# Kernel optimization log

Measured on AMD Instinct MI355X. Metric: run time of the kernel, lower is better.

Reference implementation:

```python
import jax, jax.numpy as jnp
import numpy as np

EMBED_DIM = 768
NUM_HEADS = 12
HEAD_DIM = EMBED_DIM // NUM_HEADS


def setup_inputs() -> dict:
    key = jax.random.key(0)
    k_x, k_wqkv, k_bqkv, k_wp, k_bp = jax.random.split(key, 5)
    B, S, D = 4, 2048, EMBED_DIM
    # nn.Linear default init scale ~ 1/sqrt(fan_in); exact distribution irrelevant for a reference
    lim = 1.0 / np.sqrt(D)
    x = jax.random.normal(k_x, (B, S, D), dtype=jnp.float32)
    w_qkv = jax.random.uniform(k_wqkv, (D, 3 * D), jnp.float32, -lim, lim)
    b_qkv = jax.random.uniform(k_bqkv, (3 * D,), jnp.float32, -lim, lim)
    w_proj = jax.random.uniform(k_wp, (D, D), jnp.float32, -lim, lim)
    b_proj = jax.random.uniform(k_bp, (D,), jnp.float32, -lim, lim)
    return {"x": x, "w_qkv": w_qkv, "b_qkv": b_qkv, "w_proj": w_proj, "b_proj": b_proj}


def reference(x, w_qkv, b_qkv, w_proj, b_proj):
    B, S, D = x.shape
    H, Hd = NUM_HEADS, HEAD_DIM
    qkv = x @ w_qkv + b_qkv                      # [B,S,3D]
    qkv = qkv.reshape(B, S, 3, H, Hd)
    qkv = jnp.transpose(qkv, (2, 0, 3, 1, 4))     # [3,B,H,S,Hd]
    q, k, v = qkv[0], qkv[1], qkv[2]
    scale = 1.0 / np.sqrt(Hd).astype(np.float32)
    scores = jnp.einsum("bhsd,bhtd->bhst", q, k) * scale  # [B,H,S,S]
    attn = jax.nn.softmax(scores, axis=-1)
    out = jnp.einsum("bhst,bhtd->bhsd", attn, v)  # [B,H,S,Hd]
    out = jnp.transpose(out, (0, 2, 1, 3)).reshape(B, S, D)
    return out @ w_proj + b_proj
```

## Files before the change

kernel.cpp:

```cpp
#include <hip/hip_runtime.h>


typedef _Float16 f16;
typedef _Float16 f16x8 __attribute__((ext_vector_type(8)));
typedef _Float16 f16x4 __attribute__((ext_vector_type(4)));
typedef float f32x4 __attribute__((ext_vector_type(4)));

#define BQ 4
#define SQ 2048
#define DQ 768
#define HQ 12
#define HD 64
#define M_TOK (BQ*SQ)
#define KVB 64
#define QSCALE 0.18033688f
#define THR_LOG2 11.5f

__device__ __forceinline__ void gld_lds16(const f16* g, f16* l) {
  __builtin_amdgcn_global_load_lds((const __attribute__((address_space(1))) void*)g,
                                   (__attribute__((address_space(3))) void*)l,
                                   16, 0, 0);
}

__global__ __launch_bounds__(256)
void prep(const float* __restrict__ x, f16* __restrict__ xh,
          const float* __restrict__ w_qkv, f16* __restrict__ wqkvT,
          const float* __restrict__ w_proj, f16* __restrict__ wprojT)
{
  __shared__ float tile[32][33];
  const int bid = blockIdx.x, tid = threadIdx.x;
  if (bid < 6144) {
    int i = (bid * 256 + tid) * 4;
    float4 v = *(const float4*)(x + i);
    f16x4 o = { (f16)v.x, (f16)v.y, (f16)v.z, (f16)v.w };
    *(f16x4*)(xh + i) = o;
    return;
  }
  const float* w; f16* wt; int K, N, nb, kb;
  if (bid < 7872) {
    int b2 = bid - 6144; w = w_qkv; wt = wqkvT; K = DQ; N = 3 * DQ;
    nb = (b2 % 72) * 32; kb = (b2 / 72) * 32;
  } else {
    int b3 = bid - 7872; w = w_proj; wt = wprojT; K = DQ; N = DQ;
    nb = (b3 % 24) * 32; kb = (b3 / 24) * 32;
  }
  int tx = tid & 31, ty = tid >> 5;
  for (int r = ty; r < 32; r += 8)
    tile[r][tx] = w[(size_t)(kb + r) * N + nb + tx];
  __syncthreads();
  for (int r = ty; r < 32; r += 8)
    wt[(size_t)(nb + r) * K + kb + tx] = (f16)tile[tx][r];
}

template<int MODE>
__global__ __launch_bounds__(256, 2)
void gemm128(const f16* __restrict__ A, const f16* __restrict__ Bt,
             const float* __restrict__ bias, float* __restrict__ Cf,
             f16* __restrict__ Qb, f16* __restrict__ Kb, f16* __restrict__ Vt,
             int M, int N, int K, int nbx)
{
  __shared__ f16 Ash[2][128 * 64];
  __shared__ f16 Bsh[2][128 * 64];
  const int tid = threadIdx.x;
  const int bid = blockIdx.x;
  const int nb = bid % nbx, mb = bid / nbx;
  const int m0 = mb * 128, n0 = nb * 128;
  const int lane = tid & 63, wid = tid >> 6;
  const int wr = wid >> 1, wc = wid & 1;
  const int l16 = lane & 15, l4 = lane >> 4;

  f32x4 acc[4][4] = {};

  const f16* aP[4]; const f16* bP[4]; int lOff[4];
  #pragma unroll
  for (int j = 0; j < 4; ++j) {
    int q = j * 256 + tid;
    int r = q >> 3;
    int sc = ((q & 7) ^ (r & 7)) * 8;
    aP[j] = A  + (size_t)(m0 + r) * K + sc;
    bP[j] = Bt + (size_t)(n0 + r) * K + sc;
    lOff[j] = q * 8;
  }

#define GSTAGE(buf, k0)                                   \
  do {                                                    \
    _Pragma("unroll")                                     \
    for (int j = 0; j < 4; ++j) {                         \
      gld_lds16(aP[j] + (k0), Ash[buf] + lOff[j]);        \
      gld_lds16(bP[j] + (k0), Bsh[buf] + lOff[j]);        \
    }                                                     \
  } while (0)

  GSTAGE(0, 0);
  __syncthreads();
  for (int k0 = 0; k0 < K; k0 += 64) {
    const int buf = (k0 >> 6) & 1;
    if (k0 + 64 < K) GSTAGE(buf ^ 1, k0 + 64);
    #pragma unroll
    for (int kk = 0; kk < 2; ++kk) {
      f16x8 af[4], bfr[4];
      #pragma unroll
      for (int m = 0; m < 4; ++m) {
        int R = wr * 64 + m * 16 + l16;
        af[m] = *(const f16x8*)(Ash[buf] + R * 64 + (((kk * 4 + l4) ^ (R & 7)) * 8));
      }
      #pragma unroll
      for (int n = 0; n < 4; ++n) {
        int R = wc * 64 + n * 16 + l16;
        bfr[n] = *(const f16x8*)(Bsh[buf] + R * 64 + (((kk * 4 + l4) ^ (R & 7)) * 8));
      }
      #pragma unroll
      for (int m = 0; m < 4; ++m)
        #pragma unroll
        for (int n = 0; n < 4; ++n)
          acc[m][n] = __builtin_amdgcn_mfma_f32_16x16x32_f16(af[m], bfr[n], acc[m][n], 0, 0, 0);
    }
    __syncthreads();
  }
#undef GSTAGE

  const int cbase = n0 + wc * 64;
  const int rbase = m0 + wr * 64;
  if (MODE == 1) {
    #pragma unroll
    for (int n = 0; n < 4; ++n) {
      int c = cbase + n * 16 + l16;
      float bv = bias[c];
      #pragma unroll
      for (int m = 0; m < 4; ++m)
        #pragma unroll
        for (int r = 0; r < 4; ++r) {
          int rr = rbase + m * 16 + l4 * 4 + r;
          Cf[(size_t)rr * N + c] = acc[m][n][r] + bv;
        }
    }
  } else {
    #pragma unroll
    for (int n = 0; n < 4; ++n) {
      int c = cbase + n * 16 + l16;
      float bv = bias[c];
      int which = c / DQ;
      int rem = c - which * DQ;
      int h = rem >> 6, hd = rem & 63;
      #pragma unroll
      for (int m = 0; m < 4; ++m) {
        int rr0 = rbase + m * 16 + l4 * 4;
        int b = rr0 >> 11, s = rr0 & 2047;
        size_t bh = (size_t)(b * HQ + h);
        if (which == 2) {
          f16x4 ov = { (f16)(acc[m][n][0] + bv), (f16)(acc[m][n][1] + bv),
                       (f16)(acc[m][n][2] + bv), (f16)(acc[m][n][3] + bv) };
          *(f16x4*)(Vt + (bh * HD + hd) * SQ + s) = ov;
        } else if (which == 0) {
          #pragma unroll
          for (int r = 0; r < 4; ++r)
            Qb[(bh * SQ + s + r) * HD + hd] = (f16)((acc[m][n][r] + bv) * QSCALE);
        } else {
          #pragma unroll
          for (int r = 0; r < 4; ++r)
            Kb[(bh * SQ + s + r) * HD + hd] = (f16)(acc[m][n][r] + bv);
        }
      }
    }
  }
}

__device__ __forceinline__ int permK(int p) {
  return ((p & 16) << 1) | (((p >> 2) & 3) << 3) | ((p & 32) >> 3) | (p & 3);
}

__global__ __launch_bounds__(256, 3)
void attn(const f16* __restrict__ Qb, const f16* __restrict__ Kb,
          const f16* __restrict__ Vt, f16* __restrict__ O)
{
  __shared__ f16 Ksh[2][KVB * HD];
  __shared__ f16 Vsh[2][HD * KVB];
  const int tid = threadIdx.x, lane = tid & 63, wid = tid >> 6;
  const int l16 = lane & 15, l4 = lane >> 4;

  const int nwg = gridDim.x;
  const int cpx = nwg >> 3;
  const int swz = (blockIdx.x & 7) * cpx + (blockIdx.x >> 3);
  const int qt = swz & 15, bh = swz >> 4;
  const int b = bh / HQ, h = bh - b * HQ;
  const f16* q  = Qb + (size_t)bh * SQ * HD;
  const f16* kp = Kb + (size_t)bh * SQ * HD;
  const f16* vp = Vt + (size_t)bh * HD * SQ;
  const int s0 = qt * 128 + wid * 32;

  f16x8 qf[2][2];
  #pragma unroll
  for (int g = 0; g < 2; ++g)
    #pragma unroll
    for (int kk = 0; kk < 2; ++kk)
      qf[g][kk] = *(const f16x8*)(q + (size_t)(s0 + g * 16 + l16) * HD + kk * 32 + l4 * 8);

  f32x4 oacc[2][4] = {};
  float mrun[2] = { -1e30f, -1e30f }, lrun[2] = { 0.f, 0.f };

  const int p0 = tid >> 3, p1 = (tid >> 3) + 32;
  const int scS = ((tid & 7) ^ (p0 & 7)) * 8;
  const int kr0 = permK(p0), kr1 = permK(p1);

#define STAGE(buf, t0)                                                        \
  do {                                                                        \
    gld_lds16(kp + (size_t)((t0) + kr0) * HD + scS, Ksh[buf] + tid * 8);      \
    gld_lds16(kp + (size_t)((t0) + kr1) * HD + scS, Ksh[buf] + (tid + 256) * 8);\
    gld_lds16(vp + (size_t)p0 * SQ + (t0) + scS,   Vsh[buf] + tid * 8);       \
    gld_lds16(vp + (size_t)p1 * SQ + (t0) + scS,   Vsh[buf] + (tid + 256) * 8);\
  } while (0)

#define COMPUTE(buf)                                                          \
  do {                                                                        \
    f32x4 sacc[2][4] = {};                                                    \
    __builtin_amdgcn_s_setprio(1);                                            \
    _Pragma("unroll")                                                         \
    for (int kk = 0; kk < 2; ++kk) {                                          \
      f16x8 kf[4];                                                            \
      _Pragma("unroll")                                                       \
      for (int n = 0; n < 4; ++n)                                             \
        kf[n] = *(const f16x8*)(Ksh[buf] + (n * 16 + l16) * HD +              \
                                ((kk * 32 + l4 * 8) ^ ((l16 & 7) * 8)));      \
      _Pragma("unroll")                                                       \
      for (int n = 0; n < 4; ++n) {                                           \
        sacc[0][n] = __builtin_amdgcn_mfma_f32_16x16x32_f16(kf[n], qf[0][kk], sacc[0][n], 0, 0, 0); \
        sacc[1][n] = __builtin_amdgcn_mfma_f32_16x16x32_f16(kf[n], qf[1][kk], sacc[1][n], 0, 0, 0); \
      }                                                                       \
    }                                                                         \
    __builtin_amdgcn_s_setprio(0);                                            \
    f16x8 bfr[2][2];                                                          \
    _Pragma("unroll")                                                         \
    for (int g = 0; g < 2; ++g) {                                             \
      float rm = -1e30f;                                                      \
      _Pragma("unroll")                                                       \
      for (int n = 0; n < 4; ++n)                                             \
        rm = fmaxf(rm, fmaxf(fmaxf(sacc[g][n][0], sacc[g][n][1]),             \
                             fmaxf(sacc[g][n][2], sacc[g][n][3])));           \
      rm = fmaxf(rm, __shfl_xor(rm, 16));                                     \
      rm = fmaxf(rm, __shfl_xor(rm, 32));                                     \
      if (!__all(rm - mrun[g] <= THR_LOG2)) {                                 \
        float mn = fmaxf(mrun[g], rm);                                        \
        float corr = __builtin_amdgcn_exp2f(mrun[g] - mn);                    \
        lrun[g] *= corr;                                                      \
        _Pragma("unroll")                                                     \
        for (int n = 0; n < 4; ++n)                                           \
          oacc[g][n] *= corr;                                                 \
        mrun[g] = mn;                                                         \
      }                                                                       \
      float mref = mrun[g];                                                   \
      float ps = 0.f;                                                         \
      _Pragma("unroll")                                                       \
      for (int n = 0; n < 4; ++n)                                             \
        _Pragma("unroll")                                                     \
        for (int r = 0; r < 4; ++r) {                                         \
          float pv = __builtin_amdgcn_exp2f(sacc[g][n][r] - mref);            \
          bfr[g][n & 1][(n >> 1) * 4 + r] = (f16)pv;                          \
          ps += pv;                                                           \
        }                                                                     \
      ps += __shfl_xor(ps, 16);                                               \
      ps += __shfl_xor(ps, 32);                                               \
      lrun[g] += ps;                                                          \
    }                                                                         \
    __builtin_amdgcn_s_setprio(1);                                            \
    _Pragma("unroll")                                                         \
    for (int kk = 0; kk < 2; ++kk) {                                          \
      f16x8 vf[4];                                                            \
      _Pragma("unroll")                                                       \
      for (int n = 0; n < 4; ++n)                                             \
        vf[n] = *(const f16x8*)(Vsh[buf] + (n * 16 + l16) * KVB +             \
                                ((kk * 32 + l4 * 8) ^ ((l16 & 7) * 8)));      \
      _Pragma("unroll")                                                       \
      for (int n = 0; n < 4; ++n) {                                           \
        oacc[0][n] = __builtin_amdgcn_mfma_f32_16x16x32_f16(vf[n], bfr[0][kk], oacc[0][n], 0, 0, 0); \
        oacc[1][n] = __builtin_amdgcn_mfma_f32_16x16x32_f16(vf[n], bfr[1][kk], oacc[1][n], 0, 0, 0); \
      }                                                                       \
    }                                                                         \
    __builtin_amdgcn_s_setprio(0);                                            \
  } while (0)

  STAGE(0, 0);
  __syncthreads();
  for (int t0 = 0; t0 < SQ; t0 += 2 * KVB) {
    STAGE(1, t0 + KVB);
    COMPUTE(0);
    __syncthreads();
    if (t0 + 2 * KVB < SQ) STAGE(0, t0 + 2 * KVB);
    COMPUTE(1);
    __syncthreads();
  }
#undef STAGE
#undef COMPUTE

  #pragma unroll
  for (int g = 0; g < 2; ++g) {
    float inv = 1.f / lrun[g];
    const int s = s0 + g * 16 + l16;
    f16* obase = O + ((size_t)b * SQ + s) * DQ + h * HD + l4 * 4;
    #pragma unroll
    for (int n = 0; n < 4; ++n) {
      f16x4 ov = { (f16)(oacc[g][n][0] * inv), (f16)(oacc[g][n][1] * inv),
                   (f16)(oacc[g][n][2] * inv), (f16)(oacc[g][n][3] * inv) };
      *(f16x4*)(obase + n * 16) = ov;
    }
  }
}

extern "C" void kernel_launch(void* const* d_in, const int* in_sizes, int n_in,
                              void* d_out, int out_size, void* d_ws, size_t ws_size,
                              hipStream_t stream) {
  const float* x      = (const float*)d_in[0];
  const float* w_qkv  = (const float*)d_in[1];
  const float* b_qkv  = (const float*)d_in[2];
  const float* w_proj = (const float*)d_in[3];
  const float* b_proj = (const float*)d_in[4];
  float* out = (float*)d_out;

  char* ws = (char*)d_ws;
  f16* xh     = (f16*)ws; ws += (size_t)M_TOK * DQ * 2;
  f16* wqkvT  = (f16*)ws; ws += (size_t)3 * DQ * DQ * 2;
  f16* wprojT = (f16*)ws; ws += (size_t)DQ * DQ * 2;
  f16* Qb     = (f16*)ws; ws += (size_t)M_TOK * DQ * 2;
  f16* Kb     = (f16*)ws; ws += (size_t)M_TOK * DQ * 2;
  f16* Vt     = (f16*)ws; ws += (size_t)M_TOK * DQ * 2;
  f16* AO     = xh;

  prep<<<8448, 256, 0, stream>>>(x, xh, w_qkv, wqkvT, w_proj, wprojT);

  gemm128<0><<<(M_TOK / 128) * (3 * DQ / 128), 256, 0, stream>>>(
      xh, wqkvT, b_qkv, nullptr, Qb, Kb, Vt, M_TOK, 3 * DQ, DQ, 3 * DQ / 128);

  attn<<<BQ * HQ * (SQ / 128), 256, 0, stream>>>(Qb, Kb, Vt, AO);

  gemm128<1><<<(M_TOK / 128) * (DQ / 128), 256, 0, stream>>>(
      AO, wprojT, b_proj, out, nullptr, nullptr, nullptr, M_TOK, DQ, DQ, DQ / 128);
}
```

Measured before the change: 160.0 us.

## Split attention KV range in two with a merge kernel; swizzle GEMM blocks

Attention now splits the key/value sequence into two halves, so the grid has twice as many workgroups. Each half writes partial fp32 outputs plus its running max and sum, and a new merge2 kernel combines them into the f16 output. The occupancy hint rises from 3 to 5 waves per SIMD, and the GEMM block index gets an XCD-style swizzle. This aims to fill the GPU better, but it adds a large fp32 partial write and read, an extra launch, and register pressure under the higher occupancy bound.

```diff
diff --git a/kernel.cpp b/kernel.cpp
--- a/kernel.cpp
+++ b/kernel.cpp
@@ -13,6 +13,7 @@
 #define HD 64
 #define M_TOK (BQ*SQ)
 #define KVB 64
+#define NROW (BQ*HQ*SQ)
 #define QSCALE 0.18033688f
 #define THR_LOG2 11.5f
 
@@ -62,7 +63,8 @@
   __shared__ f16 Ash[2][128 * 64];
   __shared__ f16 Bsh[2][128 * 64];
   const int tid = threadIdx.x;
-  const int bid = blockIdx.x;
+  const int cpx = gridDim.x >> 3;
+  const int bid = (blockIdx.x & 7) * cpx + (blockIdx.x >> 3);
   const int nb = bid % nbx, mb = bid / nbx;
   const int m0 = mb * 128, n0 = nb * 128;
   const int lane = tid & 63, wid = tid >> 6;
@@ -169,9 +171,11 @@
   return ((p & 16) << 1) | (((p >> 2) & 3) << 3) | ((p & 32) >> 3) | (p & 3);
 }
 
-__global__ __launch_bounds__(256, 3)
+template<int NSPLIT>
+__global__ __launch_bounds__(256, 5)
 void attn(const f16* __restrict__ Qb, const f16* __restrict__ Kb,
-          const f16* __restrict__ Vt, f16* __restrict__ O)
+          const f16* __restrict__ Vt, f16* __restrict__ O,
+          float* __restrict__ Po, float* __restrict__ Pm, float* __restrict__ Pl)
 {
   __shared__ f16 Ksh[2][KVB * HD];
   __shared__ f16 Vsh[2][HD * KVB];
@@ -181,7 +185,10 @@
   const int nwg = gridDim.x;
   const int cpx = nwg >> 3;
   const int swz = (blockIdx.x & 7) * cpx + (blockIdx.x >> 3);
-  const int qt = swz & 15, bh = swz >> 4;
+  int bh, qt, split;
+  if (NSPLIT == 2) { bh = swz >> 5; split = (swz >> 4) & 1; qt = swz & 15; }
+  else             { bh = swz >> 4; split = 0;              qt = swz & 15; }
+  const int tbase = split * (SQ / NSPLIT), tend = tbase + SQ / NSPLIT;
   const int b = bh / HQ, h = bh - b * HQ;
   const f16* q  = Qb + (size_t)bh * SQ * HD;
   const f16* kp = Kb + (size_t)bh * SQ * HD;
@@ -278,31 +285,69 @@
     __builtin_amdgcn_s_setprio(0);                                            \
   } while (0)
 
-  STAGE(0, 0);
+  STAGE(0, tbase);
   __syncthreads();
-  for (int t0 = 0; t0 < SQ; t0 += 2 * KVB) {
+  for (int t0 = tbase; t0 < tend; t0 += 2 * KVB) {
     STAGE(1, t0 + KVB);
     COMPUTE(0);
     __syncthreads();
-    if (t0 + 2 * KVB < SQ) STAGE(0, t0 + 2 * KVB);
+    if (t0 + 2 * KVB < tend) STAGE(0, t0 + 2 * KVB);
     COMPUTE(1);
     __syncthreads();
   }
 #undef STAGE
 #undef COMPUTE
 
-  #pragma unroll
-  for (int g = 0; g < 2; ++g) {
-    float inv = 1.f / lrun[g];
-    const int s = s0 + g * 16 + l16;
-    f16* obase = O + ((size_t)b * SQ + s) * DQ + h * HD + l4 * 4;
-    #pragma unroll
-    for (int n = 0; n < 4; ++n) {
-      f16x4 ov = { (f16)(oacc[g][n][0] * inv), (f16)(oacc[g][n][1] * inv),
-                   (f16)(oacc[g][n][2] * inv), (f16)(oacc[g][n][3] * inv) };
-      *(f16x4*)(obase + n * 16) = ov;
-    }
-  }
+  if (NSPLIT == 1) {
+    #pragma unroll
+    for (int g = 0; g < 2; ++g) {
+      float inv = 1.f / lrun[g];
+      const int s = s0 + g * 16 + l16;
+      f16* obase = O + ((size_t)b * SQ + s) * DQ + h * HD + l4 * 4;
+      #pragma unroll
+      for (int n = 0; n < 4; ++n) {
+        f16x4 ov = { (f16)(oacc[g][n][0] * inv), (f16)(oacc[g][n][1] * inv),
+                     (f16)(oacc[g][n][2] * inv), (f16)(oacc[g][n][3] * inv) };
+        *(f16x4*)(obase + n * 16) = ov;
+      }
+    }
+  } else {
+    #pragma unroll
+    for (int g = 0; g < 2; ++g) {
+      float inv = 1.f / lrun[g];
+      const int s = s0 + g * 16 + l16;
+      const size_t row = (size_t)split * NROW + (size_t)bh * SQ + s;
+      float* pb = Po + row * 64 + l4 * 4;
+      #pragma unroll
+      for (int n = 0; n < 4; ++n) {
+        float4 ov = { oacc[g][n][0] * inv, oacc[g][n][1] * inv,
+                      oacc[g][n][2] * inv, oacc[g][n][3] * inv };
+        *(float4*)(pb + n * 16) = ov;
+      }
+      if (l4 == 0) { Pm[row] = mrun[g]; Pl[row] = lrun[g]; }
+    }
+  }
+}
+
+__global__ __launch_bounds__(256)
+void merge2(const float* __restrict__ Po, const float* __restrict__ Pm,
+            const float* __restrict__ Pl, f16* __restrict__ AO)
+{
+  const int tid = threadIdx.x;
+  const int row = blockIdx.x * 4 + (tid >> 6);
+  const int e = tid & 63;
+  float m0 = Pm[row], m1 = Pm[row + NROW];
+  float l0 = Pl[row], l1 = Pl[row + NROW];
+  float m = fmaxf(m0, m1);
+  float w0 = l0 * __builtin_amdgcn_exp2f(m0 - m);
+  float w1 = l1 * __builtin_amdgcn_exp2f(m1 - m);
+  float inv = 1.f / (w0 + w1);
+  float o0 = Po[(size_t)row * 64 + e];
+  float o1 = Po[(size_t)(row + NROW) * 64 + e];
+  float o = (w0 * o0 + w1 * o1) * inv;
+  const int bh = row >> 11, s = row & 2047;
+  const int b = bh / HQ, h = bh - b * HQ;
+  AO[((size_t)(b * SQ + s)) * DQ + h * HD + e] = (f16)o;
 }
 
 extern "C" void kernel_launch(void* const* d_in, const int* in_sizes, int n_in,
@@ -322,14 +367,24 @@
   f16* Qb     = (f16*)ws; ws += (size_t)M_TOK * DQ * 2;
   f16* Kb     = (f16*)ws; ws += (size_t)M_TOK * DQ * 2;
   f16* Vt     = (f16*)ws; ws += (size_t)M_TOK * DQ * 2;
+  float* Po   = (float*)ws; ws += (size_t)2 * NROW * 64 * 4;
+  float* Pm   = (float*)ws; ws += (size_t)2 * NROW * 4;
+  float* Pl   = (float*)ws; ws += (size_t)2 * NROW * 4;
   f16* AO     = xh;
+
+  const bool use_split = ws_size >= (size_t)(ws - (char*)d_ws);
 
   prep<<<8448, 256, 0, stream>>>(x, xh, w_qkv, wqkvT, w_proj, wprojT);
 
   gemm128<0><<<(M_TOK / 128) * (3 * DQ / 128), 256, 0, stream>>>(
       xh, wqkvT, b_qkv, nullptr, Qb, Kb, Vt, M_TOK, 3 * DQ, DQ, 3 * DQ / 128);
 
-  attn<<<BQ * HQ * (SQ / 128), 256, 0, stream>>>(Qb, Kb, Vt, AO);
+  if (use_split) {
+    attn<2><<<BQ * HQ * (SQ / 128) * 2, 256, 0, stream>>>(Qb, Kb, Vt, AO, Po, Pm, Pl);
+    merge2<<<NROW / 4, 256, 0, stream>>>(Po, Pm, Pl, AO);
+  } else {
+    attn<1><<<BQ * HQ * (SQ / 128), 256, 0, stream>>>(Qb, Kb, Vt, AO, nullptr, nullptr, nullptr);
+  }
 
   gemm128<1><<<(M_TOK / 128) * (DQ / 128), 256, 0, stream>>>(
       AO, wprojT, b_proj, out, nullptr, nullptr, nullptr, M_TOK, DQ, DQ, DQ / 128);
```

After: 250.8 us. 56.8% more time.

## Interleave per-group softmax with PV MFMAs and swizzle GEMM block order

Applied to the files above, without the earlier changes.

The attention inner loop now loads all K and V fragments from LDS up front. It runs the softmax for group 0, issues that group's PV MFMAs, then runs group 1's softmax so it can overlap with the in-flight MFMAs instead of serializing both softmaxes before any PV work. The GEMM kernel also remaps block IDs in strides of eight, likely so neighbouring tiles land on the same XCD and share L2. The price is higher register pressure from holding kf/vf[2][4], which could hurt occupancy, and the remap assumes the grid size is a multiple of eight.

```diff
diff --git a/kernel.cpp b/kernel.cpp
--- a/kernel.cpp
+++ b/kernel.cpp
@@ -62,7 +62,8 @@
   __shared__ f16 Ash[2][128 * 64];
   __shared__ f16 Bsh[2][128 * 64];
   const int tid = threadIdx.x;
-  const int bid = blockIdx.x;
+  const int cpx = gridDim.x >> 3;
+  const int bid = (blockIdx.x & 7) * cpx + (blockIdx.x >> 3);
   const int nb = bid % nbx, mb = bid / nbx;
   const int m0 = mb * 128, n0 = nb * 128;
   const int lane = tid & 63, wid = tid >> 6;
@@ -210,71 +211,84 @@
     gld_lds16(vp + (size_t)p1 * SQ + (t0) + scS,   Vsh[buf] + (tid + 256) * 8);\
   } while (0)
 
+#define SOFTMAX(g)                                                            \
+  do {                                                                        \
+    float rm = -1e30f;                                                        \
+    _Pragma("unroll")                                                         \
+    for (int n = 0; n < 4; ++n)                                               \
+      rm = fmaxf(rm, fmaxf(fmaxf(sacc[g][n][0], sacc[g][n][1]),               \
+                           fmaxf(sacc[g][n][2], sacc[g][n][3])));             \
+    rm = fmaxf(rm, __shfl_xor(rm, 16));                                       \
+    rm = fmaxf(rm, __shfl_xor(rm, 32));                                       \
+    if (!__all(rm - mrun[g] <= THR_LOG2)) {                                   \
+      float mn = fmaxf(mrun[g], rm);                                          \
+      float corr = __builtin_amdgcn_exp2f(mrun[g] - mn);                      \
+      lrun[g] *= corr;                                                        \
+      _Pragma("unroll")                                                       \
+      for (int n = 0; n < 4; ++n)                                             \
+        oacc[g][n] *= corr;                                                   \
+      mrun[g] = mn;                                                           \
+    }                                                                         \
+    float mref = mrun[g];                                                     \
+    float ps = 0.f;                                                           \
+    _Pragma("unroll")                                                         \
+    for (int n = 0; n < 4; ++n)                                               \
+      _Pragma("unroll")                                                       \
+      for (int r = 0; r < 4; ++r) {                                           \
+        float pv = __builtin_amdgcn_exp2f(sacc[g][n][r] - mref);              \
+        bfr[g][n & 1][(n >> 1) * 4 + r] = (f16)pv;                            \
+        ps += pv;                                                             \
+      }                                                                       \
+    ps += __shfl_xor(ps, 16);                                                 \
+    ps += __shfl_xor(ps, 32);                                                 \
+    lrun[g] += ps;                                                            \
+  } while (0)
+
 #define COMPUTE(buf)                                                          \
   do {                                                                        \
     f32x4 sacc[2][4] = {};                                                    \
+    f16x8 kf[2][4];                                                           \
+    _Pragma("unroll")                                                         \
+    for (int kk = 0; kk < 2; ++kk)                                            \
+      _Pragma("unroll")                                                       \
+      for (int n = 0; n < 4; ++n)                                             \
+        kf[kk][n] = *(const f16x8*)(Ksh[buf] + (n * 16 + l16) * HD +          \
+                                    ((kk * 32 + l4 * 8) ^ ((l16 & 7) * 8)));  \
     __builtin_amdgcn_s_setprio(1);                                            \
     _Pragma("unroll")                                                         \
-    for (int kk = 0; kk < 2; ++kk) {                                          \
-      f16x8 kf[4];                                                            \
-      _Pragma("unroll")                                                       \
-      for (int n = 0; n < 4; ++n)                                             \
-        kf[n] = *(const f16x8*)(Ksh[buf] + (n * 16 + l16) * HD +              \
-                                ((kk * 32 + l4 * 8) ^ ((l16 & 7) * 8)));      \
-      _Pragma("unroll")                                                       \
-      for (int n = 0; n < 4; ++n) {                                           \
-        sacc[0][n] = __builtin_amdgcn_mfma_f32_16x16x32_f16(kf[n], qf[0][kk], sacc[0][n], 0, 0, 0); \
-        sacc[1][n] = __builtin_amdgcn_mfma_f32_16x16x32_f16(kf[n], qf[1][kk], sacc[1][n], 0, 0, 0); \
-      }                                                                       \
-    }                                                                         \
+    for (int kk = 0; kk < 2; ++kk)                                            \
+      _Pragma("unroll")                                                       \
+      for (int n = 0; n < 4; ++n)                                             \
+        sacc[0][n] = __builtin_amdgcn_mfma_f32_16x16x32_f16(kf[kk][n], qf[0][kk], sacc[0][n], 0, 0, 0); \
+    _Pragma("unroll")                                                         \
+    for (int kk = 0; kk < 2; ++kk)                                            \
+      _Pragma("unroll")                                                       \
+      for (int n = 0; n < 4; ++n)                                             \
+        sacc[1][n] = __builtin_amdgcn_mfma_f32_16x16x32_f16(kf[kk][n], qf[1][kk], sacc[1][n], 0, 0, 0); \
     __builtin_amdgcn_s_setprio(0);                                            \
+    f16x8 vf[2][4];                                                           \
+    _Pragma("unroll")                                                         \
+    for (int kk = 0; kk < 2; ++kk)                                            \
+      _Pragma("unroll")                                                       \
+      for (int n = 0; n < 4; ++n)                                             \
+        vf[kk][n] = *(const f16x8*)(Vsh[buf] + (n * 16 + l16) * KVB +         \
+                                    ((kk * 32 + l4 * 8) ^ ((l16 & 7) * 8)));  \
     f16x8 bfr[2][2];                                                          \
-    _Pragma("unroll")                                                         \
-    for (int g = 0; g < 2; ++g) {                                             \
-      float rm = -1e30f;                                                      \
-      _Pragma("unroll")                                                       \
-      for (int n = 0; n < 4; ++n)                                             \
-        rm = fmaxf(rm, fmaxf(fmaxf(sacc[g][n][0], sacc[g][n][1]),             \
-                             fmaxf(sacc[g][n][2], sacc[g][n][3])));           \
-      rm = fmaxf(rm, __shfl_xor(rm, 16));                                     \
-      rm = fmaxf(rm, __shfl_xor(rm, 32));                                     \
-      if (!__all(rm - mrun[g] <= THR_LOG2)) {                                 \
-        float mn = fmaxf(mrun[g], rm);                                        \
-        float corr = __builtin_amdgcn_exp2f(mrun[g] - mn);                    \
-        lrun[g] *= corr;                                                      \
-        _Pragma("unroll")                                                     \
-        for (int n = 0; n < 4; ++n)                                           \
-          oacc[g][n] *= corr;                                                 \
-        mrun[g] = mn;                                                         \
-      }                                                                       \
-      float mref = mrun[g];                                                   \
-      float ps = 0.f;                                                         \
-      _Pragma("unroll")                                                       \
-      for (int n = 0; n < 4; ++n)                                             \
-        _Pragma("unroll")                                                     \
-        for (int r = 0; r < 4; ++r) {                                         \
-          float pv = __builtin_amdgcn_exp2f(sacc[g][n][r] - mref);            \
-          bfr[g][n & 1][(n >> 1) * 4 + r] = (f16)pv;                          \
-          ps += pv;                                                           \
-        }                                                                     \
-      ps += __shfl_xor(ps, 16);                                               \
-      ps += __shfl_xor(ps, 32);                                               \
-      lrun[g] += ps;                                                          \
-    }                                                                         \
+    SOFTMAX(0);                    \
     __builtin_amdgcn_s_setprio(1);                                            \
     _Pragma("unroll")                                                         \
-    for (int kk = 0; kk < 2; ++kk) {                                          \
-      f16x8 vf[4];                                                            \
-      _Pragma("unroll")                                                       \
-      for (int n = 0; n < 4; ++n)                                             \
-        vf[n] = *(const f16x8*)(Vsh[buf] + (n * 16 + l16) * KVB +             \
-                                ((kk * 32 + l4 * 8) ^ ((l16 & 7) * 8)));      \
-      _Pragma("unroll")                                                       \
-      for (int n = 0; n < 4; ++n) {                                           \
-        oacc[0][n] = __builtin_amdgcn_mfma_f32_16x16x32_f16(vf[n], bfr[0][kk], oacc[0][n], 0, 0, 0); \
-        oacc[1][n] = __builtin_amdgcn_mfma_f32_16x16x32_f16(vf[n], bfr[1][kk], oacc[1][n], 0, 0, 0); \
-      }                                                                       \
-    }                                                                         \
+    for (int kk = 0; kk < 2; ++kk)                                            \
+      _Pragma("unroll")                                                       \
+      for (int n = 0; n < 4; ++n)                                             \
+        oacc[0][n] = __builtin_amdgcn_mfma_f32_16x16x32_f16(vf[kk][n], bfr[0][kk], oacc[0][n], 0, 0, 0); \
+    __builtin_amdgcn_s_setprio(0);                                            \
+    SOFTMAX(1);                             \
+    __builtin_amdgcn_s_setprio(1);                                            \
+    _Pragma("unroll")                                                         \
+    for (int kk = 0; kk < 2; ++kk)                                            \
+      _Pragma("unroll")                                                       \
+      for (int n = 0; n < 4; ++n)                                             \
+        oacc[1][n] = __builtin_amdgcn_mfma_f32_16x16x32_f16(vf[kk][n], bfr[1][kk], oacc[1][n], 0, 0, 0); \
     __builtin_amdgcn_s_setprio(0);                                            \
   } while (0)
 
@@ -290,6 +304,7 @@
   }
 #undef STAGE
 #undef COMPUTE
+#undef SOFTMAX
 
   #pragma unroll
   for (int g = 0; g < 2; ++g) {
```

New measurement: 155.6 us. -2.7%, faster.

## Halve attention query tile to 64 rows and swizzle GEMM block order across XCDs

Applied to the files above, without the earlier changes.

The attention kernel now handles 64 query rows per workgroup (16 per wave) instead of 128. That doubles the grid to 1536 blocks and raises the occupancy hint from 3 to 5 waves, with fewer registers per wave. In exchange, each K/V tile loaded into LDS is reused by half as many queries, so K/V global traffic doubles. Separately, the GEMM kernels remap block IDs with the same XCD-aware swizzle the attention kernel uses, aiming for better L2 locality.

```diff
diff --git a/kernel.cpp b/kernel.cpp
--- a/kernel.cpp
+++ b/kernel.cpp
@@ -62,7 +62,8 @@
   __shared__ f16 Ash[2][128 * 64];
   __shared__ f16 Bsh[2][128 * 64];
   const int tid = threadIdx.x;
-  const int bid = blockIdx.x;
+  const int cpx = gridDim.x >> 3;
+  const int bid = (blockIdx.x & 7) * cpx + (blockIdx.x >> 3);
   const int nb = bid % nbx, mb = bid / nbx;
   const int m0 = mb * 128, n0 = nb * 128;
   const int lane = tid & 63, wid = tid >> 6;
@@ -169,7 +170,7 @@
   return ((p & 16) << 1) | (((p >> 2) & 3) << 3) | ((p & 32) >> 3) | (p & 3);
 }
 
-__global__ __launch_bounds__(256, 3)
+__global__ __launch_bounds__(256, 5)
 void attn(const f16* __restrict__ Qb, const f16* __restrict__ Kb,
           const f16* __restrict__ Vt, f16* __restrict__ O)
 {
@@ -181,22 +182,20 @@
   const int nwg = gridDim.x;
   const int cpx = nwg >> 3;
   const int swz = (blockIdx.x & 7) * cpx + (blockIdx.x >> 3);
-  const int qt = swz & 15, bh = swz >> 4;
+  const int qt = swz & 31, bh = swz >> 5;
   const int b = bh / HQ, h = bh - b * HQ;
   const f16* q  = Qb + (size_t)bh * SQ * HD;
   const f16* kp = Kb + (size_t)bh * SQ * HD;
   const f16* vp = Vt + (size_t)bh * HD * SQ;
-  const int s0 = qt * 128 + wid * 32;
-
-  f16x8 qf[2][2];
+  const int s0 = qt * 64 + wid * 16;
+
+  f16x8 qf[2];
   #pragma unroll
-  for (int g = 0; g < 2; ++g)
-    #pragma unroll
-    for (int kk = 0; kk < 2; ++kk)
-      qf[g][kk] = *(const f16x8*)(q + (size_t)(s0 + g * 16 + l16) * HD + kk * 32 + l4 * 8);
-
-  f32x4 oacc[2][4] = {};
-  float mrun[2] = { -1e30f, -1e30f }, lrun[2] = { 0.f, 0.f };
+  for (int kk = 0; kk < 2; ++kk)
+    qf[kk] = *(const f16x8*)(q + (size_t)(s0 + l16) * HD + kk * 32 + l4 * 8);
+
+  f32x4 oacc[4] = {};
+  float mrun = -1e30f, lrun = 0.f;
 
   const int p0 = tid >> 3, p1 = (tid >> 3) + 32;
   const int scS = ((tid & 7) ^ (p0 & 7)) * 8;
@@ -212,7 +211,7 @@
 
 #define COMPUTE(buf)                                                          \
   do {                                                                        \
-    f32x4 sacc[2][4] = {};                                                    \
+    f32x4 sacc[4] = {};                                                       \
     __builtin_amdgcn_s_setprio(1);                                            \
     _Pragma("unroll")                                                         \
     for (int kk = 0; kk < 2; ++kk) {                                          \
@@ -222,45 +221,40 @@
         kf[n] = *(const f16x8*)(Ksh[buf] + (n * 16 + l16) * HD +              \
                                 ((kk * 32 + l4 * 8) ^ ((l16 & 7) * 8)));      \
       _Pragma("unroll")                                                       \
-      for (int n = 0; n < 4; ++n) {                                           \
-        sacc[0][n] = __builtin_amdgcn_mfma_f32_16x16x32_f16(kf[n], qf[0][kk], sacc[0][n], 0, 0, 0); \
-        sacc[1][n] = __builtin_amdgcn_mfma_f32_16x16x32_f16(kf[n], qf[1][kk], sacc[1][n], 0, 0, 0); \
-      }                                                                       \
+      for (int n = 0; n < 4; ++n)                                             \
+        sacc[n] = __builtin_amdgcn_mfma_f32_16x16x32_f16(kf[n], qf[kk], sacc[n], 0, 0, 0); \
     }                                                                         \
     __builtin_amdgcn_s_setprio(0);                                            \
-    f16x8 bfr[2][2];                                                          \
+    float rm = -1e30f;                                                        \
     _Pragma("unroll")                                                         \
-    for (int g = 0; g < 2; ++g) {                                             \
-      float rm = -1e30f;                                                      \
-      _Pragma("unroll")                                                       \
-      for (int n = 0; n < 4; ++n)                                             \
-        rm = fmaxf(rm, fmaxf(fmaxf(sacc[g][n][0], sacc[g][n][1]),             \
-                             fmaxf(sacc[g][n][2], sacc[g][n][3])));           \
-      rm = fmaxf(rm, __shfl_xor(rm, 16));                                     \
-      rm = fmaxf(rm, __shfl_xor(rm, 32));                                     \
-      if (!__all(rm - mrun[g] <= THR_LOG2)) {                                 \
-        float mn = fmaxf(mrun[g], rm);                                        \
-        float corr = __builtin_amdgcn_exp2f(mrun[g] - mn);                    \
-        lrun[g] *= corr;                                                      \
-        _Pragma("unroll")                                                     \
-        for (int n = 0; n < 4; ++n)                                           \
-          oacc[g][n] *= corr;                                                 \
-        mrun[g] = mn;                                                         \
+    for (int n = 0; n < 4; ++n)                                               \
+      rm = fmaxf(rm, fmaxf(fmaxf(sacc[n][0], sacc[n][1]),                     \
+                           fmaxf(sacc[n][2], sacc[n][3])));                   \
+    rm = fmaxf(rm, __shfl_xor(rm, 16));                                       \
+    rm = fmaxf(rm, __shfl_xor(rm, 32));                                       \
+    if (!__all(rm - mrun <= THR_LOG2)) {                                      \
+      float mn = fmaxf(mrun, rm);                                             \
+      float corr = __builtin_amdgcn_exp2f(mrun - mn);                         \
+      lrun *= corr;                                                           \
+      _Pragma("unroll")                                                       \
+      for (int n = 0; n < 4; ++n)                                             \
+        oacc[n] *= corr;                                                      \
+      mrun = mn;                                                              \
+    }                                                                         \
+    float mref = mrun;                                                        \
+    float ps = 0.f;                                                           \
+    f16x8 bfr[2];                                                             \
+    _Pragma("unroll")                                                         \
+    for (int n = 0; n < 4; ++n)                                               \
+      _Pragma("unroll")                                                       \
+      for (int r = 0; r < 4; ++r) {                                           \
+        float pv = __builtin_amdgcn_exp2f(sacc[n][r] - mref);                 \
+        bfr[n & 1][(n >> 1) * 4 + r] = (f16)pv;                               \
+        ps += pv;                                                             \
       }                                                                       \
-      float mref = mrun[g];                                                   \
-      float ps = 0.f;                                                         \
-      _Pragma("unroll")                                                       \
-      for (int n = 0; n < 4; ++n)                                             \
-        _Pragma("unroll")                                                     \
-        for (int r = 0; r < 4; ++r) {                                         \
-          float pv = __builtin_amdgcn_exp2f(sacc[g][n][r] - mref);            \
-          bfr[g][n & 1][(n >> 1) * 4 + r] = (f16)pv;                          \
-          ps += pv;                                                           \
-        }                                                                     \
-      ps += __shfl_xor(ps, 16);                                               \
-      ps += __shfl_xor(ps, 32);                                               \
-      lrun[g] += ps;                                                          \
-    }                                                                         \
+    ps += __shfl_xor(ps, 16);                                                 \
+    ps += __shfl_xor(ps, 32);                                                 \
+    lrun += ps;                                                               \
     __builtin_amdgcn_s_setprio(1);                                            \
     _Pragma("unroll")                                                         \
     for (int kk = 0; kk < 2; ++kk) {                                          \
@@ -270,10 +264,8 @@
         vf[n] = *(const f16x8*)(Vsh[buf] + (n * 16 + l16) * KVB +             \
                                 ((kk * 32 + l4 * 8) ^ ((l16 & 7) * 8)));      \
       _Pragma("unroll")                                                       \
-      for (int n = 0; n < 4; ++n) {                                           \
-        oacc[0][n] = __builtin_amdgcn_mfma_f32_16x16x32_f16(vf[n], bfr[0][kk], oacc[0][n], 0, 0, 0); \
-        oacc[1][n] = __builtin_amdgcn_mfma_f32_16x16x32_f16(vf[n], bfr[1][kk], oacc[1][n], 0, 0, 0); \
-      }                                                                       \
+      for (int n = 0; n < 4; ++n)                                             \
+        oacc[n] = __builtin_amdgcn_mfma_f32_16x16x32_f16(vf[n], bfr[kk], oacc[n], 0, 0, 0); \
     }                                                                         \
     __builtin_amdgcn_s_setprio(0);                                            \
   } while (0)
@@ -291,15 +283,14 @@
 #undef STAGE
 #undef COMPUTE
 
-  #pragma unroll
-  for (int g = 0; g < 2; ++g) {
-    float inv = 1.f / lrun[g];
-    const int s = s0 + g * 16 + l16;
+  {
+    float inv = 1.f / lrun;
+    const int s = s0 + l16;
     f16* obase = O + ((size_t)b * SQ + s) * DQ + h * HD + l4 * 4;
     #pragma unroll
     for (int n = 0; n < 4; ++n) {
-      f16x4 ov = { (f16)(oacc[g][n][0] * inv), (f16)(oacc[g][n][1] * inv),
-                   (f16)(oacc[g][n][2] * inv), (f16)(oacc[g][n][3] * inv) };
+      f16x4 ov = { (f16)(oacc[n][0] * inv), (f16)(oacc[n][1] * inv),
+                   (f16)(oacc[n][2] * inv), (f16)(oacc[n][3] * inv) };
       *(f16x4*)(obase + n * 16) = ov;
     }
   }
@@ -329,7 +320,7 @@
   gemm128<0><<<(M_TOK / 128) * (3 * DQ / 128), 256, 0, stream>>>(
       xh, wqkvT, b_qkv, nullptr, Qb, Kb, Vt, M_TOK, 3 * DQ, DQ, 3 * DQ / 128);
 
-  attn<<<BQ * HQ * (SQ / 128), 256, 0, stream>>>(Qb, Kb, Vt, AO);
+  attn<<<BQ * HQ * (SQ / 64), 256, 0, stream>>>(Qb, Kb, Vt, AO);
 
   gemm128<1><<<(M_TOK / 128) * (DQ / 128), 256, 0, stream>>>(
       AO, wprojT, b_proj, out, nullptr, nullptr, nullptr, M_TOK, DQ, DQ, DQ / 128);
```

New measurement: 167.3 us. 1.05x slower.
